# Kernel optimization log

Hardware: AMD Instinct MI355X
Metric: run time of the kernel (lower is better)

The kernel has to match this reference:

```python
import jax, jax.numpy as jnp
import numpy as np

B, N, L, D, V = 32, 2048, 128, 1024, 32000

def setup_inputs() -> dict:
    key = jax.random.key(0)
    k1, k2, k3 = jax.random.split(key, 3)
    image_features = jax.random.normal(k1, (B, N, D), dtype=jnp.float32)
    token_ids = jax.random.randint(k2, (B, L), 0, V, dtype=jnp.int64)
    emb_table = jax.random.normal(k3, (V, D), dtype=jnp.float32)
    return {"image_features": image_features, "token_ids": token_ids, "emb_table": emb_table}

def reference(image_features, token_ids, emb_table):
    # targets = embeddings(input_ids): [B, L, D]
    targets = emb_table[token_ids]
    # batched pairwise L2 distance (torch.cdist p=2): ||x-y|| via the
    # expanded form ||x||^2 + ||y||^2 - 2<x,y>, clamped for numerical safety.
    x2 = jnp.sum(image_features * image_features, axis=-1)        # [B, N]
    y2 = jnp.sum(targets * targets, axis=-1)                      # [B, L]
    xy = jnp.einsum('bnd,bld->bnl', image_features, targets)      # [B, N, L]
    d2 = x2[:, :, None] + y2[:, None, :] - 2.0 * xy
    costs = jnp.sqrt(jnp.maximum(d2, 0.0))                        # [B, N, L]
    smallest = jnp.min(costs, axis=-1)                            # [B, N]
    return smallest.mean()
```

## Files before the change

### kernel.cpp

```cpp
#include <hip/hip_runtime.h>
#include <cstdint>
#include <cstddef>

#define BATCH 32
#define NROW  2048
#define LTOK  128
#define DDIM  1024

#define BM    128
#define BK    64
#define LDST  72

typedef short s8v  __attribute__((ext_vector_type(8)));
typedef float f4v  __attribute__((ext_vector_type(4)));

__device__ __forceinline__ uint32_t pk2(float lo, float hi) {
    return __builtin_amdgcn_perm(__float_as_uint(hi), __float_as_uint(lo), 0x07060302u);
}

__global__ __launch_bounds__(256)
void prep_y(const int*   __restrict__ tok,
            const float* __restrict__ E,
            uint32_t*    __restrict__ Ybf,
            float*       __restrict__ y2)
{
    const int l = blockIdx.x, b = blockIdx.y;
    const int tid = threadIdx.x;
    const int t = tok[b * LTOK + l];
    const float4 v = ((const float4*)(E + (size_t)t * DDIM))[tid];
    float s = v.x*v.x + v.y*v.y + v.z*v.z + v.w*v.w;
    uint2 p; p.x = pk2(v.x, v.y); p.y = pk2(v.z, v.w);
    ((uint2*)(Ybf + ((size_t)(b * LTOK + l) * DDIM) / 2))[tid] = p;
#pragma unroll
    for (int o = 1; o < 64; o <<= 1) s += __shfl_xor(s, o);
    __shared__ float ws4[4];
    if ((tid & 63) == 0) ws4[tid >> 6] = s;
    __syncthreads();
    if (tid == 0) y2[b * LTOK + l] = ws4[0] + ws4[1] + ws4[2] + ws4[3];
}

__global__ __launch_bounds__(256, 2)
void cdist_min_mean_kernel(const float* __restrict__ X,
                           const short* __restrict__ Ybf,
                           const float* __restrict__ y2g,
                           float* __restrict__ out)
{
    __shared__ __align__(16) short Xs[BM * LDST];
    __shared__ __align__(16) short Ys[LTOK * 64];
    __shared__ float x2s[BM];
    __shared__ float rowmin[BM * 2];
    __shared__ float wsum[4];

    const int tid  = threadIdx.x;
    const int lane = tid & 63;
    const int wid  = tid >> 6;
    const int grp  = tid >> 3;
    const int sub  = tid & 7;

    const int b       = blockIdx.y;
    const int rowBase = blockIdx.x * BM;

    const float* Xg = X + ((size_t)b * NROW + rowBase) * DDIM;

    const float* xp[4];
#pragma unroll
    for (int i = 0; i < 4; ++i)
        xp[i] = Xg + (size_t)(grp + 32 * i) * DDIM + sub * 8;

    const short* yg[4];
#pragma unroll
    for (int it = 0; it < 4; ++it) {
        int c   = it * 256 + tid;
        int row = c >> 3;
        int chs = (c & 7) ^ (row & 7);
        yg[it] = Ybf + (size_t)(b * LTOK + row) * DDIM + chs * 8;
    }

    f4v acc[4][4];
#pragma unroll
    for (int mi = 0; mi < 4; ++mi)
#pragma unroll
        for (int ni = 0; ni < 4; ++ni)
            acc[mi][ni] = (f4v){0.f, 0.f, 0.f, 0.f};

    float xacc[4] = {0.f, 0.f, 0.f, 0.f};

    const int quad = lane >> 4;
    const int l15  = lane & 15;
    const int wm   = wid >> 1;
    const int wn   = wid & 1;

    for (int k0 = 0; k0 < DDIM; k0 += BK) {
        float4 xa[4], xb[4];
#pragma unroll
        for (int i = 0; i < 4; ++i) {
            xa[i] = *(const float4*)(xp[i] + k0);
            xb[i] = *(const float4*)(xp[i] + k0 + 4);
        }
        __syncthreads();

#pragma unroll
        for (int it = 0; it < 4; ++it)
            __builtin_amdgcn_global_load_lds(
                (const __attribute__((address_space(1))) void*)(yg[it] + k0),
                (__attribute__((address_space(3))) void*)&Ys[(it * 256 + (wid << 6)) * 8],
                16, 0, 0);

#pragma unroll
        for (int i = 0; i < 4; ++i) {
            const float4 a = xa[i], c4 = xb[i];
            xacc[i] += a.x*a.x + a.y*a.y + a.z*a.z + a.w*a.w
                     + c4.x*c4.x + c4.y*c4.y + c4.z*c4.z + c4.w*c4.w;
            uint4 p;
            p.x = pk2(a.x, a.y);  p.y = pk2(a.z, a.w);
            p.z = pk2(c4.x, c4.y); p.w = pk2(c4.z, c4.w);
            *(uint4*)&Xs[(grp + 32 * i) * LDST + sub * 8] = p;
        }
        __syncthreads();

#pragma unroll
        for (int ks = 0; ks < BK; ks += 32) {
            s8v af[4], bfr[4];
#pragma unroll
            for (int mi = 0; mi < 4; ++mi)
                af[mi] = *(const s8v*)&Xs[(wm * 64 + mi * 16 + l15) * LDST + ks + quad * 8];
#pragma unroll
            for (int ni = 0; ni < 4; ++ni) {
                int brow = wn * 64 + ni * 16 + l15;
                int ch   = ((ks >> 3) + quad) ^ (brow & 7);
                bfr[ni]  = *(const s8v*)&Ys[brow * 64 + ch * 8];
            }
#pragma unroll
            for (int mi = 0; mi < 4; ++mi)
#pragma unroll
                for (int ni = 0; ni < 4; ++ni)
                    acc[mi][ni] = __builtin_amdgcn_mfma_f32_16x16x32_bf16(
                        af[mi], bfr[ni], acc[mi][ni], 0, 0, 0);
        }
    }

#pragma unroll
    for (int i = 0; i < 4; ++i) {
        float s = xacc[i];
        s += __shfl_xor(s, 1); s += __shfl_xor(s, 2); s += __shfl_xor(s, 4);
        if ((lane & 7) == 0) x2s[grp + 32 * i] = s;
    }
    __syncthreads();

    float y2r[4];
#pragma unroll
    for (int ni = 0; ni < 4; ++ni)
        y2r[ni] = y2g[b * LTOK + wn * 64 + ni * 16 + l15];

#pragma unroll
    for (int mi = 0; mi < 4; ++mi) {
#pragma unroll
        for (int j = 0; j < 4; ++j) {
            float m = y2r[0] - 2.f * acc[mi][0][j];
            m = fminf(m, y2r[1] - 2.f * acc[mi][1][j]);
            m = fminf(m, y2r[2] - 2.f * acc[mi][2][j]);
            m = fminf(m, y2r[3] - 2.f * acc[mi][3][j]);
            m = fminf(m, __shfl_xor(m, 1));
            m = fminf(m, __shfl_xor(m, 2));
            m = fminf(m, __shfl_xor(m, 4));
            m = fminf(m, __shfl_xor(m, 8));
            if (l15 == 0)
                rowmin[(wm * 64 + mi * 16 + quad * 4 + j) * 2 + wn] = m;
        }
    }
    __syncthreads();

    float part = 0.f;
    if (tid < BM) {
        float m = fminf(rowmin[tid * 2], rowmin[tid * 2 + 1]);
        part = sqrtf(fmaxf(x2s[tid] + m, 0.f));
    }
#pragma unroll
    for (int s = 1; s < 64; s <<= 1) part += __shfl_xor(part, s);
    if (lane == 0) wsum[wid] = part;
    __syncthreads();
    if (tid == 0) {
        float tot = (wsum[0] + wsum[1] + wsum[2] + wsum[3])
                  * (1.0f / (float)(BATCH * NROW));
        atomicAdd(out, tot);
    }
}

extern "C" void kernel_launch(void* const* d_in, const int* in_sizes, int n_in,
                              void* d_out, int out_size, void* d_ws, size_t ws_size,
                              hipStream_t stream) {
    const float* X   = (const float*)d_in[0];
    const int*   tok = (const int*)d_in[1];
    const float* E   = (const float*)d_in[2];
    float* out = (float*)d_out;

    uint32_t* Ybf = (uint32_t*)d_ws;
    float*    y2  = (float*)((char*)d_ws + (size_t)BATCH * LTOK * DDIM * 2);

    hipMemsetAsync(out, 0, sizeof(float), stream);

    dim3 pgrid(LTOK, BATCH, 1);
    prep_y<<<pgrid, 256, 0, stream>>>(tok, E, Ybf, y2);

    dim3 grid(NROW / BM, BATCH, 1);
    cdist_min_mean_kernel<<<grid, 256, 0, stream>>>(X, (const short*)Ybf, y2, out);
}
```

Measured before the change: 441.0 us.

## Halve row tile, double-buffer X in LDS, load Y fragments directly to registers

Shrinks the row tile from 128 to 64 so twice as many blocks launch with higher occupancy. X tiles are double-buffered in LDS and prefetched two steps ahead, which leaves one barrier per K step. Y bf16 fragments are no longer staged through LDS; each wave loads its MFMA B operands straight from global memory into registers. The trade-off is that Y is re-read from global/L2 by more blocks and by both wave rows, and the final reduction now does one atomic per wave.

```diff
diff --git a/kernel.cpp b/kernel.cpp
--- a/kernel.cpp
+++ b/kernel.cpp
@@ -7,8 +7,9 @@
 #define LTOK  128
 #define DDIM  1024
 
-#define BM    128
+#define BM    64
 #define BK    64
+#define NK    (DDIM / BK)
 #define LDST  72
 
 typedef short s8v  __attribute__((ext_vector_type(8)));
@@ -39,17 +40,15 @@
     if (tid == 0) y2[b * LTOK + l] = ws4[0] + ws4[1] + ws4[2] + ws4[3];
 }
 
-__global__ __launch_bounds__(256, 2)
+__global__ __launch_bounds__(256, 4)
 void cdist_min_mean_kernel(const float* __restrict__ X,
                            const short* __restrict__ Ybf,
                            const float* __restrict__ y2g,
                            float* __restrict__ out)
 {
-    __shared__ __align__(16) short Xs[BM * LDST];
-    __shared__ __align__(16) short Ys[LTOK * 64];
+    __shared__ __align__(16) short Xs[2][BM * LDST];
     __shared__ float x2s[BM];
     __shared__ float rowmin[BM * 2];
-    __shared__ float wsum[4];
 
     const int tid  = threadIdx.x;
     const int lane = tid & 63;
@@ -60,92 +59,92 @@
     const int b       = blockIdx.y;
     const int rowBase = blockIdx.x * BM;
 
-    const float* Xg = X + ((size_t)b * NROW + rowBase) * DDIM;
-
-    const float* xp[4];
-#pragma unroll
-    for (int i = 0; i < 4; ++i)
-        xp[i] = Xg + (size_t)(grp + 32 * i) * DDIM + sub * 8;
-
-    const short* yg[4];
-#pragma unroll
-    for (int it = 0; it < 4; ++it) {
-        int c   = it * 256 + tid;
-        int row = c >> 3;
-        int chs = (c & 7) ^ (row & 7);
-        yg[it] = Ybf + (size_t)(b * LTOK + row) * DDIM + chs * 8;
-    }
-
-    f4v acc[4][4];
-#pragma unroll
-    for (int mi = 0; mi < 4; ++mi)
-#pragma unroll
-        for (int ni = 0; ni < 4; ++ni)
-            acc[mi][ni] = (f4v){0.f, 0.f, 0.f, 0.f};
-
-    float xacc[4] = {0.f, 0.f, 0.f, 0.f};
+    const float* Xg  = X + ((size_t)b * NROW + rowBase) * DDIM;
+    const float* xp0 = Xg + (size_t)grp * DDIM + sub * 8;
+    const float* xp1 = Xg + (size_t)(grp + 32) * DDIM + sub * 8;
 
     const int quad = lane >> 4;
     const int l15  = lane & 15;
     const int wm   = wid >> 1;
     const int wn   = wid & 1;
 
-    for (int k0 = 0; k0 < DDIM; k0 += BK) {
-        float4 xa[4], xb[4];
-#pragma unroll
-        for (int i = 0; i < 4; ++i) {
-            xa[i] = *(const float4*)(xp[i] + k0);
-            xb[i] = *(const float4*)(xp[i] + k0 + 4);
+    const short* yb[4];
+#pragma unroll
+    for (int ni = 0; ni < 4; ++ni)
+        yb[ni] = Ybf + (size_t)(b * LTOK + wn * 64 + ni * 16 + l15) * DDIM + quad * 8;
+
+    f4v acc[2][4];
+#pragma unroll
+    for (int mi = 0; mi < 2; ++mi)
+#pragma unroll
+        for (int ni = 0; ni < 4; ++ni)
+            acc[mi][ni] = (f4v){0.f, 0.f, 0.f, 0.f};
+
+    float xacc[2] = {0.f, 0.f};
+
+    float4 xra[2], xrb[2];
+    s8v    yr[4][2];
+
+    auto loadx = [&](int k) {
+        xra[0] = *(const float4*)(xp0 + k * BK);
+        xrb[0] = *(const float4*)(xp0 + k * BK + 4);
+        xra[1] = *(const float4*)(xp1 + k * BK);
+        xrb[1] = *(const float4*)(xp1 + k * BK + 4);
+    };
+    auto loady = [&](int k) {
+#pragma unroll
+        for (int ni = 0; ni < 4; ++ni)
+#pragma unroll
+            for (int s = 0; s < 2; ++s)
+                yr[ni][s] = *(const s8v*)(yb[ni] + k * BK + s * 32);
+    };
+    auto pack = [&](int dst) {
+#pragma unroll
+        for (int i = 0; i < 2; ++i) {
+            const float4 a = xra[i], c = xrb[i];
+            xacc[i] += a.x*a.x + a.y*a.y + a.z*a.z + a.w*a.w
+                     + c.x*c.x + c.y*c.y + c.z*c.z + c.w*c.w;
+            uint4 p;
+            p.x = pk2(a.x, a.y); p.y = pk2(a.z, a.w);
+            p.z = pk2(c.x, c.y); p.w = pk2(c.z, c.w);
+            *(uint4*)&Xs[dst][(grp + 32 * i) * LDST + sub * 8] = p;
         }
-        __syncthreads();
-
-#pragma unroll
-        for (int it = 0; it < 4; ++it)
-            __builtin_amdgcn_global_load_lds(
-                (const __attribute__((address_space(1))) void*)(yg[it] + k0),
-                (__attribute__((address_space(3))) void*)&Ys[(it * 256 + (wid << 6)) * 8],
-                16, 0, 0);
-
-#pragma unroll
-        for (int i = 0; i < 4; ++i) {
-            const float4 a = xa[i], c4 = xb[i];
-            xacc[i] += a.x*a.x + a.y*a.y + a.z*a.z + a.w*a.w
-                     + c4.x*c4.x + c4.y*c4.y + c4.z*c4.z + c4.w*c4.w;
-            uint4 p;
-            p.x = pk2(a.x, a.y);  p.y = pk2(a.z, a.w);
-            p.z = pk2(c4.x, c4.y); p.w = pk2(c4.z, c4.w);
-            *(uint4*)&Xs[(grp + 32 * i) * LDST + sub * 8] = p;
-        }
-        __syncthreads();
-
-#pragma unroll
-        for (int ks = 0; ks < BK; ks += 32) {
-            s8v af[4], bfr[4];
-#pragma unroll
-            for (int mi = 0; mi < 4; ++mi)
-                af[mi] = *(const s8v*)&Xs[(wm * 64 + mi * 16 + l15) * LDST + ks + quad * 8];
-#pragma unroll
-            for (int ni = 0; ni < 4; ++ni) {
-                int brow = wn * 64 + ni * 16 + l15;
-                int ch   = ((ks >> 3) + quad) ^ (brow & 7);
-                bfr[ni]  = *(const s8v*)&Ys[brow * 64 + ch * 8];
-            }
-#pragma unroll
-            for (int mi = 0; mi < 4; ++mi)
+    };
+
+    loadx(0);
+    pack(0);
+    loadx(1);
+    loady(0);
+    __syncthreads();
+
+#pragma unroll
+    for (int k = 0; k < NK; ++k) {
+        const int buf = k & 1;
+        if (k < NK - 1) pack(buf ^ 1);
+        if (k < NK - 2) loadx(k + 2);
+#pragma unroll
+        for (int ks = 0; ks < 2; ++ks) {
+            s8v af[2];
+#pragma unroll
+            for (int mi = 0; mi < 2; ++mi)
+                af[mi] = *(const s8v*)&Xs[buf][(wm * 32 + mi * 16 + l15) * LDST + ks * 32 + quad * 8];
+#pragma unroll
+            for (int mi = 0; mi < 2; ++mi)
 #pragma unroll
                 for (int ni = 0; ni < 4; ++ni)
                     acc[mi][ni] = __builtin_amdgcn_mfma_f32_16x16x32_bf16(
-                        af[mi], bfr[ni], acc[mi][ni], 0, 0, 0);
+                        af[mi], yr[ni][ks], acc[mi][ni], 0, 0, 0);
         }
-    }
-
-#pragma unroll
-    for (int i = 0; i < 4; ++i) {
+        if (k < NK - 1) loady(k + 1);
+        __syncthreads();
+    }
+
+#pragma unroll
+    for (int i = 0; i < 2; ++i) {
         float s = xacc[i];
         s += __shfl_xor(s, 1); s += __shfl_xor(s, 2); s += __shfl_xor(s, 4);
         if ((lane & 7) == 0) x2s[grp + 32 * i] = s;
     }
-    __syncthreads();
 
     float y2r[4];
 #pragma unroll
@@ -153,7 +152,7 @@
         y2r[ni] = y2g[b * LTOK + wn * 64 + ni * 16 + l15];
 
 #pragma unroll
-    for (int mi = 0; mi < 4; ++mi) {
+    for (int mi = 0; mi < 2; ++mi) {
 #pragma unroll
         for (int j = 0; j < 4; ++j) {
             float m = y2r[0] - 2.f * acc[mi][0][j];
@@ -165,24 +164,18 @@
             m = fminf(m, __shfl_xor(m, 4));
             m = fminf(m, __shfl_xor(m, 8));
             if (l15 == 0)
-                rowmin[(wm * 64 + mi * 16 + quad * 4 + j) * 2 + wn] = m;
+                rowmin[(wm * 32 + mi * 16 + quad * 4 + j) * 2 + wn] = m;
         }
     }
     __syncthreads();
 
-    float part = 0.f;
     if (tid < BM) {
         float m = fminf(rowmin[tid * 2], rowmin[tid * 2 + 1]);
-        part = sqrtf(fmaxf(x2s[tid] + m, 0.f));
-    }
-#pragma unroll
-    for (int s = 1; s < 64; s <<= 1) part += __shfl_xor(part, s);
-    if (lane == 0) wsum[wid] = part;
-    __syncthreads();
-    if (tid == 0) {
-        float tot = (wsum[0] + wsum[1] + wsum[2] + wsum[3])
-                  * (1.0f / (float)(BATCH * NROW));
-        atomicAdd(out, tot);
+        float part = sqrtf(fmaxf(x2s[tid] + m, 0.f));
+#pragma unroll
+        for (int s = 1; s < 64; s <<= 1) part += __shfl_xor(part, s);
+        if (lane == 0)
+            atomicAdd(out, part * (1.0f / (float)(BATCH * NROW)));
     }
 }
 
```

Result: slower. 466.3 us (+5.7%).
